# Kernel optimization log

Hardware: AMD Instinct MI355X
Metric: run time of the kernel (lower is better)

## Reference

```python
import jax, jax.numpy as jnp
import numpy as np

D = 128   # node feature dim
C = 2     # classes
N = 50000 # nodes
E = 500000  # edges (before self-loops)
H1 = 2    # conv1 heads
NEG_SLOPE = 0.2
BN_EPS = 1e-5


def setup_inputs() -> dict:
    key = jax.random.key(0)
    ks = jax.random.split(key, 24)
    rn = lambda k, shape, s=0.05: jax.random.normal(k, shape, dtype=jnp.float32) * s
    inp = {
        'x': jax.random.normal(ks[0], (N, D), dtype=jnp.float32),
        'edge_index': jax.random.randint(ks[1], (2, E), 0, N, dtype=jnp.int64),
        # conv1: GATConv(D, D, heads=2, concat=True)
        'W1': rn(ks[2], (D, H1 * D)),
        'att_src1': rn(ks[3], (H1, D)),
        'att_dst1': rn(ks[4], (H1, D)),
        'bias1': jnp.zeros((H1 * D,), jnp.float32),
        # conv2: GATConv(2D, D, heads=1, concat=False)
        'W2': rn(ks[5], (2 * D, D)),
        'att_src2': rn(ks[6], (1, D)),
        'att_dst2': rn(ks[7], (1, D)),
        'bias2': jnp.zeros((D,), jnp.float32),
        # lin1 = MLP([3D, 96]) : Linear -> ReLU -> BatchNorm1d
        'Wl': rn(ks[8], (3 * D, 96)), 'bl': jnp.zeros((96,), jnp.float32),
        'gl': jnp.ones((96,), jnp.float32), 'betal': jnp.zeros((96,), jnp.float32),
        # mlp1 = MLP([96, 96, C]) : two (Linear -> ReLU -> BN) blocks
        'Wa': rn(ks[9], (96, 96)), 'ba': jnp.zeros((96,), jnp.float32),
        'ga': jnp.ones((96,), jnp.float32), 'betaa': jnp.zeros((96,), jnp.float32),
        'Wb': rn(ks[10], (96, C)), 'bb': jnp.zeros((C,), jnp.float32),
        'gb': jnp.ones((C,), jnp.float32), 'betab': jnp.zeros((C,), jnp.float32),
    }
    return inp


def gat_conv(x, src, dst, W, att_src, att_dst, bias, heads, out_dim, concat):
    # PyG GATConv: h = x W -> [N,H,F]; per-edge logit leakyrelu(a_s.h_src + a_d.h_dst);
    # segment softmax over edges grouped by destination; weighted scatter-sum.
    n = x.shape[0]
    h = (x @ W).reshape(n, heads, out_dim)
    a_src = jnp.einsum('nhd,hd->nh', h, att_src)  # [N,H]
    a_dst = jnp.einsum('nhd,hd->nh', h, att_dst)
    alpha = jax.nn.leaky_relu(a_src[src] + a_dst[dst], NEG_SLOPE)  # [Etot,H]
    m = jax.ops.segment_max(alpha, dst, num_segments=n)            # [N,H]
    e = jnp.exp(alpha - m[dst])
    s = jax.ops.segment_sum(e, dst, num_segments=n)
    w = e / (s[dst] + 1e-16)                                       # [Etot,H]
    out = jax.ops.segment_sum(h[src] * w[:, :, None], dst, num_segments=n)  # [N,H,F]
    out = out.reshape(n, heads * out_dim) if concat else out.mean(axis=1)
    return out + bias


def mlp_block(x, W, b, gamma, beta):
    # Linear -> ReLU -> BatchNorm1d (training-mode batch stats, biased var)
    y = jax.nn.relu(x @ W + b)
    mu = y.mean(axis=0)
    var = ((y - mu) ** 2).mean(axis=0)
    return gamma * (y - mu) / jnp.sqrt(var + BN_EPS) + beta


def reference(x, edge_index, W1, att_src1, att_dst1, bias1,
              W2, att_src2, att_dst2, bias2,
              Wl, bl, gl, betal, Wa, ba, ga, betaa, Wb, bb, gb, betab):
    n = x.shape[0]
    # PyG GATConv default add_self_loops=True
    loops = jnp.arange(n, dtype=edge_index.dtype)
    src = jnp.concatenate([edge_index[0], loops])
    dst = jnp.concatenate([edge_index[1], loops])
    x1 = gat_conv(x, src, dst, W1, att_src1, att_dst1, bias1, H1, D, True)    # [N,2D]
    x2 = gat_conv(x1, src, dst, W2, att_src2, att_dst2, bias2, 1, D, False)   # [N,D]
    h = jnp.concatenate([x1, x2], axis=1)                                      # [N,3D]
    h = mlp_block(h, Wl, bl, gl, betal)     # lin1
    h = mlp_block(h, Wa, ba, ga, betaa)     # mlp1 layer 1
    h = mlp_block(h, Wb, bb, gb, betab)     # mlp1 layer 2
    return h
```

## Files before the change

### kernel.cpp

```cpp
#include <hip/hip_runtime.h>
#include <hip/hip_bf16.h>
#include <cstdint>
#include <cstddef>

#define NNODES 50000
#define NEDGES 500000
#define ETOT   (NEDGES + NNODES)

typedef __attribute__((ext_vector_type(8))) short short8;
typedef __attribute__((ext_vector_type(8))) unsigned short ushort8v;
typedef __attribute__((ext_vector_type(4))) float floatx4;
typedef __attribute__((ext_vector_type(4))) unsigned short ushort4v;

__device__ __forceinline__ unsigned short f2bf(float f) {
    union { __hip_bfloat16 h; unsigned short u; } cv;
    cv.h = __float2bfloat16(f);
    return cv.u;
}
__device__ __forceinline__ float bf2f(unsigned short u) {
    union { unsigned int i; float f; } cv;
    cv.i = ((unsigned int)u) << 16;
    return cv.f;
}

#define GBM 128
#define GBN 64
#define GBK 32

__global__ __launch_bounds__(256, 4) void gemm_mfma(
    const unsigned short* __restrict__ A, int lda,
    const unsigned short* __restrict__ Bt,
    float* __restrict__ C,
    unsigned short* __restrict__ Cb, int ldc,
    const float* __restrict__ bias,
    float* __restrict__ colsum, float* __restrict__ colsq,
    int M, int N, int K, int do_relu)
{
    __shared__ __attribute__((aligned(16))) unsigned short Alds[GBM * GBK];
    __shared__ __attribute__((aligned(16))) unsigned short Blds[GBN * GBK];
    __shared__ float scol[GBN], sqcol[GBN];

    int tid = threadIdx.x;
    int wave = tid >> 6, lane = tid & 63;
    int row0 = blockIdx.y * GBM;
    int col0 = blockIdx.x * GBN;
    int m = lane & 15, q = lane >> 4;

    floatx4 acc[2][4] = {};

    for (int k0 = 0; k0 < K; k0 += GBK) {
        #pragma unroll
        for (int i = 0; i < 2; ++i) {
            int c = tid + i * 256;
            int r = c >> 2, off = (c & 3) * 8;
            int gr = row0 + r;
            short8 v = {};
            if (gr < M) v = *(const short8*)(A + (size_t)gr * lda + k0 + off);
            *(short8*)(Alds + r * GBK + off) = v;
        }
        {
            int r = tid >> 2, off = (tid & 3) * 8;
            short8 v = *(const short8*)(Bt + (size_t)(col0 + r) * K + k0 + off);
            *(short8*)(Blds + r * GBK + off) = v;
        }
        __syncthreads();

        short8 a0 = *(const short8*)(Alds + (wave * 32 + m) * GBK + q * 8);
        short8 a1 = *(const short8*)(Alds + (wave * 32 + 16 + m) * GBK + q * 8);
        #pragma unroll
        for (int ct = 0; ct < 4; ++ct) {
            short8 b = *(const short8*)(Blds + (ct * 16 + m) * GBK + q * 8);
            acc[0][ct] = __builtin_amdgcn_mfma_f32_16x16x32_bf16(a0, b, acc[0][ct], 0, 0, 0);
            acc[1][ct] = __builtin_amdgcn_mfma_f32_16x16x32_bf16(a1, b, acc[1][ct], 0, 0, 0);
        }
        __syncthreads();
    }

    float ps[4] = {}, pq[4] = {};
    #pragma unroll
    for (int rt = 0; rt < 2; ++rt) {
        #pragma unroll
        for (int r = 0; r < 4; ++r) {
            int gr = row0 + wave * 32 + rt * 16 + q * 4 + r;
            #pragma unroll
            for (int ct = 0; ct < 4; ++ct) {
                int gc = col0 + ct * 16 + m;
                float v = acc[rt][ct][r];
                if (gc < N) {
                    float vb = v;
                    if (bias != nullptr) vb += bias[gc];
                    if (do_relu) vb = fmaxf(vb, 0.f);
                    if (gr < M) {
                        if (C  != nullptr) C[(size_t)gr * ldc + gc] = vb;
                        if (Cb != nullptr) Cb[(size_t)gr * ldc + gc] = f2bf(vb);
                        ps[ct] += vb; pq[ct] += vb * vb;
                    }
                }
            }
        }
    }
    if (colsum != nullptr) {
        if (tid < GBN) { scol[tid] = 0.f; sqcol[tid] = 0.f; }
        __syncthreads();
        #pragma unroll
        for (int ct = 0; ct < 4; ++ct) {
            atomicAdd(&scol[ct * 16 + m], ps[ct]);
            atomicAdd(&sqcol[ct * 16 + m], pq[ct]);
        }
        __syncthreads();
        if (tid < GBN) {
            int gc = col0 + tid;
            if (gc < N) {
                atomicAdd(&colsum[gc], scol[tid]);
                atomicAdd(&colsq[gc], sqcol[tid]);
            }
        }
    }
}

__global__ __launch_bounds__(256) void fold_cast_zero(
    const float* __restrict__ W1, const float* __restrict__ as1v, const float* __restrict__ ad1v,
    const float* __restrict__ W2, const float* __restrict__ as2v, const float* __restrict__ ad2v,
    const float* __restrict__ Wl,
    float* __restrict__ U1, float* __restrict__ U2,
    unsigned short* __restrict__ W1t, unsigned short* __restrict__ W2t,
    unsigned short* __restrict__ Wlt,
    int* __restrict__ rowst, float* __restrict__ as2z, float* __restrict__ statz)
{
    int z = blockIdx.x * 256 + threadIdx.x;
    if (z <= NNODES) rowst[z] = 0;
    if (z < 2 * NNODES) as2z[z] = 0.f;
    if (z < 1536) statz[z] = 0.f;

    if (blockIdx.x < 64) {
        int g = threadIdx.x >> 5, l = threadIdx.x & 31;
        int task = blockIdx.x * 8 + g;
        float ss = 0.f, sd = 0.f;
        if (task < 256) {
            int d = task & 127, h = task >> 7;
            const float4 wv = *(const float4*)(W1 + d * 256 + h * 128 + l * 4);
            const float4 av = *(const float4*)(as1v + h * 128 + l * 4);
            const float4 bv = *(const float4*)(ad1v + h * 128 + l * 4);
            ss = wv.x * av.x + wv.y * av.y + wv.z * av.z + wv.w * av.w;
            sd = wv.x * bv.x + wv.y * bv.y + wv.z * bv.z + wv.w * bv.w;
        } else {
            int k = task - 256;
            const float4 wv = *(const float4*)(W2 + (size_t)k * 128 + l * 4);
            const float4 av = *(const float4*)(as2v + l * 4);
            const float4 bv = *(const float4*)(ad2v + l * 4);
            ss = wv.x * av.x + wv.y * av.y + wv.z * av.z + wv.w * av.w;
            sd = wv.x * bv.x + wv.y * bv.y + wv.z * bv.z + wv.w * bv.w;
        }
        #pragma unroll
        for (int off = 1; off < 32; off <<= 1) { ss += __shfl_xor(ss, off); sd += __shfl_xor(sd, off); }
        if (l == 0) {
            if (task < 256) {
                int d = task & 127, h = task >> 7;
                U1[h * 128 + d] = ss;
                U1[256 + h * 128 + d] = sd;
            } else {
                int k = task - 256;
                U2[k] = ss;
                U2[256 + k] = sd;
            }
        }
    } else {
        int i = (blockIdx.x - 64) * 256 + threadIdx.x;
        if (i < 32768) {
            int n = i >> 7, k = i & 127;
            W1t[i] = f2bf(W1[k * 256 + n]);
        } else if (i < 65536) {
            int j = i - 32768;
            int n = j >> 8, k = j & 255;
            W2t[j] = f2bf(W2[k * 128 + n]);
        } else if (i < 114688) {
            int j = i - 65536;
            int n = j / 384, k = j % 384;
            Wlt[j] = (n < 96) ? f2bf(Wl[(size_t)k * 96 + n]) : (unsigned short)0;
        }
    }
}

__device__ __forceinline__ void edge_src_dst(const int* ei, int e, int& src, int& dst) {
    if (e < NEDGES) { src = ei[e]; dst = ei[NEDGES + e]; }
    else { src = e - NEDGES; dst = src; }
}

#define CASTB ((NNODES + 7) / 8)
#define EDGEB ((ETOT + 255) / 256)

__global__ __launch_bounds__(256) void cast_csr(
    const float* __restrict__ x, const float* __restrict__ U1,
    unsigned short* __restrict__ xb, float* __restrict__ as1, float* __restrict__ ad1,
    const int* __restrict__ ei, int* __restrict__ cnt)
{
    __shared__ float Us[512];
    int tid = threadIdx.x;
    if (blockIdx.x < CASTB) {
        Us[tid] = U1[tid];
        Us[tid + 256] = U1[tid + 256];
        __syncthreads();
        int g = tid >> 5, l = tid & 31;
        int n = blockIdx.x * 8 + g;
        if (n >= NNODES) return;
        const float4 v = *(const float4*)(x + (size_t)n * 128 + l * 4);
        ushort4v o;
        o.x = f2bf(v.x); o.y = f2bf(v.y); o.z = f2bf(v.z); o.w = f2bf(v.w);
        *(ushort4v*)(xb + (size_t)n * 128 + l * 4) = o;
        const float4 us0 = *(const float4*)(Us + l * 4);
        const float4 us1 = *(const float4*)(Us + 128 + l * 4);
        const float4 ud0 = *(const float4*)(Us + 256 + l * 4);
        const float4 ud1 = *(const float4*)(Us + 384 + l * 4);
        float s0 = v.x * us0.x + v.y * us0.y + v.z * us0.z + v.w * us0.w;
        float s1 = v.x * us1.x + v.y * us1.y + v.z * us1.z + v.w * us1.w;
        float d0 = v.x * ud0.x + v.y * ud0.y + v.z * ud0.z + v.w * ud0.w;
        float d1 = v.x * ud1.x + v.y * ud1.y + v.z * ud1.z + v.w * ud1.w;
        #pragma unroll
        for (int off = 1; off < 32; off <<= 1) {
            s0 += __shfl_xor(s0, off); s1 += __shfl_xor(s1, off);
            d0 += __shfl_xor(d0, off); d1 += __shfl_xor(d1, off);
        }
        if (l == 0) {
            as1[n * 2] = s0; as1[n * 2 + 1] = s1;
            ad1[n * 2] = d0; ad1[n * 2 + 1] = d1;
        }
    } else {
        int e = (blockIdx.x - CASTB) * 256 + tid;
        if (e >= ETOT) return;
        int src, dst; edge_src_dst(ei, e, src, dst); (void)src;
        atomicAdd(&cnt[dst], 1);
    }
}

__global__ void bnfold_a(const float* __restrict__ csum, const float* __restrict__ csq,
                         const float* __restrict__ gamma, const float* __restrict__ beta,
                         const float* __restrict__ Wa, const float* __restrict__ ba,
                         unsigned short* __restrict__ Wat2, float* __restrict__ ba_f) {
    __shared__ float scl[96], shf[96];
    int tid = threadIdx.x;
    if (tid < 96) {
        float mu  = csum[tid] / (float)NNODES;
        float var = csq[tid] / (float)NNODES - mu * mu;
        if (var < 0.f) var = 0.f;
        float sc = gamma[tid] * rsqrtf(var + 1e-5f);
        scl[tid] = sc; shf[tid] = beta[tid] - mu * sc;
    }
    __syncthreads();
    for (int idx = tid; idx < 128 * 96; idx += 256) {
        int n = idx / 96, k = idx % 96;
        Wat2[idx] = (n < 96) ? f2bf(scl[k] * Wa[k * 96 + n]) : (unsigned short)0;
    }
    if (tid < 96) {
        float s = ba[tid];
        for (int k = 0; k < 96; ++k) s += shf[k] * Wa[k * 96 + tid];
        ba_f[tid] = s;
    }
}

__global__ void bnfold_b(const float* __restrict__ csum, const float* __restrict__ csq,
                         const float* __restrict__ gamma, const float* __restrict__ beta,
                         const float* __restrict__ Wb, const float* __restrict__ bb,
                         unsigned short* __restrict__ Wbt, float* __restrict__ bb_f) {
    __shared__ float scl[96], shf[96];
    int tid = threadIdx.x;
    if (tid < 96) {
        float mu  = csum[tid] / (float)NNODES;
        float var = csq[tid] / (float)NNODES - mu * mu;
        if (var < 0.f) var = 0.f;
        float sc = gamma[tid] * rsqrtf(var + 1e-5f);
        scl[tid] = sc; shf[tid] = beta[tid] - mu * sc;
    }
    __syncthreads();
    for (int idx = tid; idx < 64 * 96; idx += 256) {
        int n = idx / 96, k = idx % 96;
        Wbt[idx] = (n < 2) ? f2bf(scl[k] * Wb[k * 2 + n]) : (unsigned short)0;
    }
    if (tid < 2) {
        float s = bb[tid];
        for (int k = 0; k < 96; ++k) s += shf[k] * Wb[k * 2 + tid];
        bb_f[tid] = s;
    }
}

__global__ void bn_fin_apply(const float* __restrict__ csum, const float* __restrict__ csq,
                             const float* __restrict__ gamma, const float* __restrict__ beta,
                             float* __restrict__ y, int total) {
    int i = blockIdx.x * blockDim.x + threadIdx.x;
    if (i >= total) return;
    int j = i & 1;
    float mu  = csum[j] / (float)NNODES;
    float var = csq[j] / (float)NNODES - mu * mu;
    if (var < 0.f) var = 0.f;
    float sc = gamma[j] * rsqrtf(var + 1e-5f);
    float sh = beta[j] - mu * sc;
    y[i] = y[i] * sc + sh;
}

#define SCAN_CH 1024
#define SCAN_NB ((NNODES + SCAN_CH - 1) / SCAN_CH)

__global__ __launch_bounds__(256) void scan1(const int* __restrict__ cnt, int* __restrict__ part) {
    int t = threadIdx.x;
    int base = blockIdx.x * SCAN_CH + t * 4;
    int4 v = {0, 0, 0, 0};
    if (base + 3 < NNODES) v = *(const int4*)(cnt + base);
    else {
        if (base + 0 < NNODES) v.x = cnt[base + 0];
        if (base + 1 < NNODES) v.y = cnt[base + 1];
        if (base + 2 < NNODES) v.z = cnt[base + 2];
        if (base + 3 < NNODES) v.w = cnt[base + 3];
    }
    int s = v.x + v.y + v.z + v.w;
    __shared__ int sm[256];
    sm[t] = s;
    __syncthreads();
    for (int off = 128; off > 0; off >>= 1) {
        if (t < off) sm[t] += sm[t + off];
        __syncthreads();
    }
    if (t == 0) part[blockIdx.x] = sm[0];
}

__global__ __launch_bounds__(256) void scan23(const int* __restrict__ cnt, const int* __restrict__ part,
                                              int* __restrict__ rowstart, int* __restrict__ cursor) {
    __shared__ int sbase;
    int t = threadIdx.x;
    if (t < 64) {
        int v = (t < SCAN_NB) ? part[t] : 0;
        #pragma unroll
        for (int off = 1; off < 64; off <<= 1) {
            int u = __shfl_up(v, off);
            if (t >= off) v += u;
        }
        int ex = __shfl_up(v, 1);
        if (t == 0) ex = 0;
        if (t == (int)blockIdx.x) sbase = ex;
        if (blockIdx.x == 0 && t == 0) rowstart[NNODES] = ETOT;
    }
    int base = blockIdx.x * SCAN_CH + t * 4;
    int4 v = {0, 0, 0, 0};
    if (base + 3 < NNODES) v = *(const int4*)(cnt + base);
    else {
        if (base + 0 < NNODES) v.x = cnt[base + 0];
        if (base + 1 < NNODES) v.y = cnt[base + 1];
        if (base + 2 < NNODES) v.z = cnt[base + 2];
        if (base + 3 < NNODES) v.w = cnt[base + 3];
    }
    int s = v.x + v.y + v.z + v.w;
    __shared__ int sm[2][256];
    sm[0][t] = s;
    __syncthreads();
    int cur = 0;
    #pragma unroll
    for (int off = 1; off < 256; off <<= 1) {
        int nxt = cur ^ 1;
        int val = sm[cur][t];
        if (t >= off) val += sm[cur][t - off];
        sm[nxt][t] = val;
        __syncthreads();
        cur = nxt;
    }
    int p = sm[cur][t] - s + sbase;
    if (base + 0 < NNODES) { rowstart[base + 0] = p; cursor[base + 0] = p; } p += v.x;
    if (base + 1 < NNODES) { rowstart[base + 1] = p; cursor[base + 1] = p; } p += v.y;
    if (base + 2 < NNODES) { rowstart[base + 2] = p; cursor[base + 2] = p; } p += v.z;
    if (base + 3 < NNODES) { rowstart[base + 3] = p; cursor[base + 3] = p; }
}

__global__ __launch_bounds__(256) void csr_fill(const int* __restrict__ ei,
                                                int* __restrict__ cursor,
                                                int* __restrict__ esrc) {
    int e = blockIdx.x * blockDim.x + threadIdx.x;
    if (e >= ETOT) return;
    int src, dst; edge_src_dst(ei, e, src, dst);
    int pos = atomicAdd(&cursor[dst], 1);
    esrc[pos] = src;
}

__global__ __launch_bounds__(256, 4) void gat_conv1_fused(
    const int* __restrict__ rowstart, const int* __restrict__ esrc,
    const unsigned short* __restrict__ xb, const float* __restrict__ a_src,
    const float* __restrict__ a_dst, const unsigned short* __restrict__ W1t,
    const float* __restrict__ bias1, const float* __restrict__ U2,
    unsigned short* __restrict__ xcat, float* __restrict__ as2, float* __restrict__ ad2)
{
    __shared__ __attribute__((aligned(16))) unsigned short Alds[16 * 264];
    __shared__ float U2s[512];
    __shared__ float Bs[256];

    int tid = threadIdx.x;
    int t = tid & 15;
    int g = tid >> 4;
    int nb = blockIdx.x * 16;
    int n = nb + g;

    U2s[tid] = U2[tid];
    U2s[tid + 256] = U2[tid + 256];
    Bs[tid] = bias1[tid];

    int beg = rowstart[n], deg = rowstart[n + 1] - beg;
    const float2 adv = *(const float2*)(a_dst + (size_t)n * 2);
    float acc0[8] = {}, acc1[8] = {};

    if (deg <= 32) {
        int sa = 0, sb = 0;
        float la0 = -1e30f, la1 = -1e30f;
        float lb0 = -1e30f, lb1 = -1e30f;
        if (t < deg) {
            sa = esrc[beg + t];
            const float2 asv = *(const float2*)(a_src + (size_t)sa * 2);
            la0 = asv.x + adv.x; la0 = la0 >= 0.f ? la0 : 0.2f * la0;
            lb0 = asv.y + adv.y; lb0 = lb0 >= 0.f ? lb0 : 0.2f * lb0;
        }
        if (t + 16 < deg) {
            sb = esrc[beg + 16 + t];
            const float2 asv = *(const float2*)(a_src + (size_t)sb * 2);
            la1 = asv.x + adv.x; la1 = la1 >= 0.f ? la1 : 0.2f * la1;
            lb1 = asv.y + adv.y; lb1 = lb1 >= 0.f ? lb1 : 0.2f * lb1;
        }
        float m0 = fmaxf(la0, la1), m1 = fmaxf(lb0, lb1);
        #pragma unroll
        for (int off = 1; off < 16; off <<= 1) {
            m0 = fmaxf(m0, __shfl_xor(m0, off, 16));
            m1 = fmaxf(m1, __shfl_xor(m1, off, 16));
        }
        float ea0 = (t < deg)      ? __expf(la0 - m0) : 0.f;
        float ea1 = (t + 16 < deg) ? __expf(la1 - m0) : 0.f;
        float eb0 = (t < deg)      ? __expf(lb0 - m1) : 0.f;
        float eb1 = (t + 16 < deg) ? __expf(lb1 - m1) : 0.f;
        float s0 = ea0 + ea1, s1 = eb0 + eb1;
        #pragma unroll
        for (int off = 1; off < 16; off <<= 1) {
            s0 += __shfl_xor(s0, off, 16);
            s1 += __shfl_xor(s1, off, 16);
        }
        float i0 = 1.f / (s0 + 1e-16f), i1 = 1.f / (s1 + 1e-16f);
        float wa0 = ea0 * i0, wa1 = ea1 * i0;
        float wb0 = eb0 * i1, wb1 = eb1 * i1;

        int e = 0;
        for (; e + 3 < deg; e += 4) {
            int sx[4]; float w0x[4], w1x[4];
            #pragma unroll
            for (int u = 0; u < 4; ++u) {
                int ee = e + u;
                int hi = ee & 16, ln = ee & 15;
                sx[u]  = __shfl(hi ? sb  : sa,  ln, 16);
                w0x[u] = __shfl(hi ? wa1 : wa0, ln, 16);
                w1x[u] = __shfl(hi ? wb1 : wb0, ln, 16);
            }
            ushort8v hv[4];
            #pragma unroll
            for (int u = 0; u < 4; ++u)
                hv[u] = *(const ushort8v*)(xb + (size_t)sx[u] * 128 + t * 8);
            #pragma unroll
            for (int u = 0; u < 4; ++u) {
                #pragma unroll
                for (int j = 0; j < 8; ++j) {
                    float f = bf2f(hv[u][j]);
                    acc0[j] += w0x[u] * f;
                    acc1[j] += w1x[u] * f;
                }
            }
        }
        for (; e < deg; ++e) {
            int hi = e & 16, ln = e & 15;
            int   sX  = __shfl(hi ? sb  : sa,  ln, 16);
            float wX0 = __shfl(hi ? wa1 : wa0, ln, 16);
            float wX1 = __shfl(hi ? wb1 : wb0, ln, 16);
            const ushort8v hv = *(const ushort8v*)(xb + (size_t)sX * 128 + t * 8);
            #pragma unroll
            for (int j = 0; j < 8; ++j) {
                float f = bf2f(hv[j]);
                acc0[j] += wX0 * f; acc1[j] += wX1 * f;
            }
        }
    } else {
        float m0 = -1e30f, m1 = -1e30f;
        for (int idx = t; idx < deg; idx += 16) {
            int s = esrc[beg + idx];
            const float2 asv = *(const float2*)(a_src + (size_t)s * 2);
            float l0 = asv.x + adv.x; l0 = l0 >= 0.f ? l0 : 0.2f * l0;
            float l1 = asv.y + adv.y; l1 = l1 >= 0.f ? l1 : 0.2f * l1;
            m0 = fmaxf(m0, l0); m1 = fmaxf(m1, l1);
        }
        #pragma unroll
        for (int off = 1; off < 16; off <<= 1) {
            m0 = fmaxf(m0, __shfl_xor(m0, off, 16));
            m1 = fmaxf(m1, __shfl_xor(m1, off, 16));
        }
        float s0 = 0.f, s1 = 0.f;
        for (int idx = t; idx < deg; idx += 16) {
            int s = esrc[beg + idx];
            const float2 asv = *(const float2*)(a_src + (size_t)s * 2);
            float l0 = asv.x + adv.x; l0 = l0 >= 0.f ? l0 : 0.2f * l0;
            float l1 = asv.y + adv.y; l1 = l1 >= 0.f ? l1 : 0.2f * l1;
            s0 += __expf(l0 - m0); s1 += __expf(l1 - m1);
        }
        #pragma unroll
        for (int off = 1; off < 16; off <<= 1) {
            s0 += __shfl_xor(s0, off, 16);
            s1 += __shfl_xor(s1, off, 16);
        }
        float inv0 = 1.f / (s0 + 1e-16f), inv1 = 1.f / (s1 + 1e-16f);
        for (int e = 0; e < deg; ++e) {
            int s = esrc[beg + e];
            const float2 asv = *(const float2*)(a_src + (size_t)s * 2);
            float l0 = asv.x + adv.x; l0 = l0 >= 0.f ? l0 : 0.2f * l0;
            float l1 = asv.y + adv.y; l1 = l1 >= 0.f ? l1 : 0.2f * l1;
            float w0 = __expf(l0 - m0) * inv0, w1 = __expf(l1 - m1) * inv1;
            const ushort8v hv = *(const ushort8v*)(xb + (size_t)s * 128 + t * 8);
            #pragma unroll
            for (int j = 0; j < 8; ++j) {
                float f = bf2f(hv[j]);
                acc0[j] += w0 * f; acc1[j] += w1 * f;
            }
        }
    }

    {
        ushort8v o0, o1;
        #pragma unroll
        for (int j = 0; j < 8; ++j) { o0[j] = f2bf(acc0[j]); o1[j] = f2bf(acc1[j]); }
        *(ushort8v*)(Alds + g * 264 + t * 8) = o0;
        *(ushort8v*)(Alds + g * 264 + 128 + t * 8) = o1;
    }
    __syncthreads();

    int wave = tid >> 6, lane = tid & 63;
    int m = lane & 15, q = lane >> 4;
    int ncol0 = wave * 64;
    int kbase = (wave >= 2) ? 128 : 0;

    floatx4 cacc[4] = {};
    #pragma unroll
    for (int ks = 0; ks < 4; ++ks) {
        short8 a = *(const short8*)(Alds + m * 264 + kbase + ks * 32 + q * 8);
        #pragma unroll
        for (int ct = 0; ct < 4; ++ct) {
            short8 b = *(const short8*)(W1t + (size_t)(ncol0 + ct * 16 + m) * 128 + ks * 32 + q * 8);
            cacc[ct] = __builtin_amdgcn_mfma_f32_16x16x32_bf16(a, b, cacc[ct], 0, 0, 0);
        }
    }

    #pragma unroll
    for (int r = 0; r < 4; ++r) {
        int row = q * 4 + r;
        int gn = nb + row;
        float ds = 0.f, dd = 0.f;
        #pragma unroll
        for (int ct = 0; ct < 4; ++ct) {
            int col = ncol0 + ct * 16 + m;
            float vb = cacc[ct][r] + Bs[col];
            ds += vb * U2s[col];
            dd += vb * U2s[256 + col];
            xcat[(size_t)gn * 384 + col] = f2bf(vb);
        }
        #pragma unroll
        for (int off = 1; off < 16; off <<= 1) {
            ds += __shfl_xor(ds, off);
            dd += __shfl_xor(dd, off);
        }
        if (m == 0) {
            atomicAdd(&as2[gn], ds);
            atomicAdd(&ad2[gn], dd);
        }
    }
}

__global__ __launch_bounds__(256) void gat_gather_h1(
    const int* __restrict__ rowstart, const int* __restrict__ esrc,
    const unsigned short* __restrict__ hb, const float* __restrict__ a_src,
    const float* __restrict__ a_dst, const float* __restrict__ bias,
    unsigned short* __restrict__ xcat)
{
    int tid = threadIdx.x;
    int t = tid & 15;
    int g0 = (blockIdx.x * blockDim.x + tid) >> 4;
    int gstride = (gridDim.x * blockDim.x) >> 4;

    for (int n = g0; n < NNODES; n += gstride) {
        int beg = rowstart[n], deg = rowstart[n + 1] - beg;
        float ad0 = a_dst[n];
        float acc[8] = {};

        if (deg <= 32) {
            int sa = 0, sb = 0;
            float l0 = -1e30f, l1 = -1e30f;
            if (t < deg) {
                sa = esrc[beg + t];
                l0 = a_src[sa] + ad0; l0 = l0 >= 0.f ? l0 : 0.2f * l0;
            }
            if (t + 16 < deg) {
                sb = esrc[beg + 16 + t];
                l1 = a_src[sb] + ad0; l1 = l1 >= 0.f ? l1 : 0.2f * l1;
            }
            float m0 = fmaxf(l0, l1);
            #pragma unroll
            for (int off = 1; off < 16; off <<= 1)
                m0 = fmaxf(m0, __shfl_xor(m0, off, 16));
            float e0 = (t < deg)      ? __expf(l0 - m0) : 0.f;
            float e1 = (t + 16 < deg) ? __expf(l1 - m0) : 0.f;
            float s0 = e0 + e1;
            #pragma unroll
            for (int off = 1; off < 16; off <<= 1)
                s0 += __shfl_xor(s0, off, 16);
            float i0 = 1.f / (s0 + 1e-16f);
            float w0 = e0 * i0, w1 = e1 * i0;

            int e = 0;
            for (; e + 3 < deg; e += 4) {
                int sx[4]; float wx[4];
                #pragma unroll
                for (int u = 0; u < 4; ++u) {
                    int ee = e + u;
                    int hi = ee & 16, ln = ee & 15;
                    sx[u] = __shfl(hi ? sb : sa, ln, 16);
                    wx[u] = __shfl(hi ? w1 : w0, ln, 16);
                }
                ushort8v hv[4];
                #pragma unroll
                for (int u = 0; u < 4; ++u)
                    hv[u] = *(const ushort8v*)(hb + (size_t)sx[u] * 128 + t * 8);
                #pragma unroll
                for (int u = 0; u < 4; ++u) {
                    #pragma unroll
                    for (int j = 0; j < 8; ++j)
                        acc[j] += wx[u] * bf2f(hv[u][j]);
                }
            }
            for (; e < deg; ++e) {
                int hi = e & 16, ln = e & 15;
                int   sX = __shfl(hi ? sb : sa, ln, 16);
                float wX = __shfl(hi ? w1 : w0, ln, 16);
                const ushort8v hv = *(const ushort8v*)(hb + (size_t)sX * 128 + t * 8);
                #pragma unroll
                for (int j = 0; j < 8; ++j) acc[j] += wX * bf2f(hv[j]);
            }
        } else {
            float m0 = -1e30f;
            for (int idx = t; idx < deg; idx += 16) {
                int s = esrc[beg + idx];
                float l = a_src[s] + ad0; l = l >= 0.f ? l : 0.2f * l;
                m0 = fmaxf(m0, l);
            }
            #pragma unroll
            for (int off = 1; off < 16; off <<= 1)
                m0 = fmaxf(m0, __shfl_xor(m0, off, 16));
            float s0 = 0.f;
            for (int idx = t; idx < deg; idx += 16) {
                int s = esrc[beg + idx];
                float l = a_src[s] + ad0; l = l >= 0.f ? l : 0.2f * l;
                s0 += __expf(l - m0);
            }
            #pragma unroll
            for (int off = 1; off < 16; off <<= 1)
                s0 += __shfl_xor(s0, off, 16);
            float inv0 = 1.f / (s0 + 1e-16f);
            for (int e = 0; e < deg; ++e) {
                int s = esrc[beg + e];
                float l = a_src[s] + ad0; l = l >= 0.f ? l : 0.2f * l;
                float w = __expf(l - m0) * inv0;
                const ushort8v hv = *(const ushort8v*)(hb + (size_t)s * 128 + t * 8);
                #pragma unroll
                for (int j = 0; j < 8; ++j) acc[j] += w * bf2f(hv[j]);
            }
        }

        const float4 b0 = *(const float4*)(bias + t * 8);
        const float4 b1 = *(const float4*)(bias + t * 8 + 4);
        ushort8v o;
        o[0] = f2bf(acc[0] + b0.x); o[1] = f2bf(acc[1] + b0.y);
        o[2] = f2bf(acc[2] + b0.z); o[3] = f2bf(acc[3] + b0.w);
        o[4] = f2bf(acc[4] + b1.x); o[5] = f2bf(acc[5] + b1.y);
        o[6] = f2bf(acc[6] + b1.z); o[7] = f2bf(acc[7] + b1.w);
        *(ushort8v*)(xcat + (size_t)n * 384 + 256 + t * 8) = o;
    }
}

extern "C" void kernel_launch(void* const* d_in, const int* in_sizes, int n_in,
                              void* d_out, int out_size, void* d_ws, size_t ws_size,
                              hipStream_t stream) {
    const float* x        = (const float*)d_in[0];
    const int*   ei       = (const int*)d_in[1];
    const float* W1       = (const float*)d_in[2];
    const float* att_src1 = (const float*)d_in[3];
    const float* att_dst1 = (const float*)d_in[4];
    const float* bias1    = (const float*)d_in[5];
    const float* W2       = (const float*)d_in[6];
    const float* att_src2 = (const float*)d_in[7];
    const float* att_dst2 = (const float*)d_in[8];
    const float* bias2    = (const float*)d_in[9];
    const float* Wl       = (const float*)d_in[10];
    const float* bl       = (const float*)d_in[11];
    const float* gl       = (const float*)d_in[12];
    const float* betal    = (const float*)d_in[13];
    const float* Wa       = (const float*)d_in[14];
    const float* ba       = (const float*)d_in[15];
    const float* ga       = (const float*)d_in[16];
    const float* betaa    = (const float*)d_in[17];
    const float* Wb       = (const float*)d_in[18];
    const float* bb       = (const float*)d_in[19];
    const float* gb       = (const float*)d_in[20];
    const float* betab    = (const float*)d_in[21];
    float* out = (float*)d_out;
    char* ws = (char*)d_ws;

    const int N = NNODES;

    const size_t offY2b  = 0;
    const size_t offXcat = 19200000;
    const size_t offXb   = 57600000;
    const size_t offY1b  = 70400000;
    const size_t offW1t  = 105600000;
    const size_t offW2t  = 105665536;
    const size_t offWlt  = 105731072;
    const size_t offWat2 = 105829376;
    const size_t offWbt  = 105853952;
    const size_t offBaf  = 105866240;
    const size_t offBbf  = 105866640;
    const size_t offU1   = 105867264;
    const size_t offU2   = 105869312;
    const size_t offRow  = 106000000;
    const size_t offCur  = 106200128;
    const size_t offEsrc = 106400832;
    const size_t offPart = 108700000;
    const size_t offAs1  = 108800000;
    const size_t offAd1  = 109200000;
    const size_t offAs2  = 109600000;
    const size_t offAd2  = 109800000;
    const size_t offSt   = 110000000;

    unsigned short* y2b   = (unsigned short*)(ws + offY2b);
    unsigned short* xcat  = (unsigned short*)(ws + offXcat);
    unsigned short* xb    = (unsigned short*)(ws + offXb);
    unsigned short* hb2   = (unsigned short*)(ws + offXb);
    unsigned short* y1b   = (unsigned short*)(ws + offY1b);
    unsigned short* W1t   = (unsigned short*)(ws + offW1t);
    unsigned short* W2t   = (unsigned short*)(ws + offW2t);
    unsigned short* Wlt   = (unsigned short*)(ws + offWlt);
    unsigned short* Wat2  = (unsigned short*)(ws + offWat2);
    unsigned short* Wbt   = (unsigned short*)(ws + offWbt);
    float* ba_f = (float*)(ws + offBaf);
    float* bb_f = (float*)(ws + offBbf);
    float* U1   = (float*)(ws + offU1);
    float* U2   = (float*)(ws + offU2);
    int* rowst  = (int*)(ws + offRow);
    int* cursor = (int*)(ws + offCur);
    int* esrc   = (int*)(ws + offEsrc);
    int* part   = (int*)(ws + offPart);
    float* as1  = (float*)(ws + offAs1);
    float* ad1  = (float*)(ws + offAd1);
    float* as2  = (float*)(ws + offAs2);
    float* ad2  = (float*)(ws + offAd2);
    float* statz = (float*)(ws + offSt);

    float* csum_l = (float*)(ws + offSt + 0);
    float* csq_l  = (float*)(ws + offSt + 512);
    float* csum_a = (float*)(ws + offSt + 2048);
    float* csq_a  = (float*)(ws + offSt + 2560);
    float* csum_b = (float*)(ws + offSt + 4096);
    float* csq_b  = (float*)(ws + offSt + 4608);

    dim3 blk(256);
    int gatherBlocks = 2048;
    dim3 gemmRows((N + GBM - 1) / GBM);

    fold_cast_zero<<<512, blk, 0, stream>>>(W1, att_src1, att_dst1, W2, att_src2, att_dst2,
                                            Wl, U1, U2, W1t, W2t, Wlt, rowst, as2, statz);

    cast_csr<<<CASTB + EDGEB, blk, 0, stream>>>(x, U1, xb, as1, ad1, ei, rowst);

    scan1<<<SCAN_NB, blk, 0, stream>>>(rowst, part);
    scan23<<<SCAN_NB, blk, 0, stream>>>(rowst, part, rowst, cursor);
    csr_fill<<<EDGEB, blk, 0, stream>>>(ei, cursor, esrc);

    gat_conv1_fused<<<NNODES / 16, blk, 0, stream>>>(
        rowst, esrc, xb, as1, ad1, W1t, bias1, U2, xcat, as2, ad2);

    gemm_mfma<<<dim3(2, gemmRows.x), blk, 0, stream>>>(
        xcat, 384, W2t, nullptr, hb2, 128, nullptr, nullptr, nullptr,
        N, 128, 256, 0);
    gat_gather_h1<<<gatherBlocks, blk, 0, stream>>>(rowst, esrc, hb2, as2, ad2, bias2, xcat);

    gemm_mfma<<<dim3(2, gemmRows.x), blk, 0, stream>>>(
        xcat, 384, Wlt, nullptr, y1b, 96, bl, csum_l, csq_l,
        N, 96, 384, 1);
    bnfold_a<<<1, 256, 0, stream>>>(csum_l, csq_l, gl, betal, Wa, ba, Wat2, ba_f);

    gemm_mfma<<<dim3(2, gemmRows.x), blk, 0, stream>>>(
        y1b, 96, Wat2, nullptr, y2b, 96, ba_f, csum_a, csq_a,
        N, 96, 96, 1);
    bnfold_b<<<1, 256, 0, stream>>>(csum_a, csq_a, ga, betaa, Wb, bb, Wbt, bb_f);

    gemm_mfma<<<dim3(1, gemmRows.x), blk, 0, stream>>>(
        y2b, 96, Wbt, out, nullptr, 2, bb_f, csum_b, csq_b,
        N, 2, 96, 1);

    bn_fin_apply<<<(N * 2 + 255) / 256, blk, 0, stream>>>(csum_b, csq_b, gb, betab, out, N * 2);
}
```

Measured before the change: 344.7 us.

## Fuse BN fold and final BN apply into GEMM last-block tails

Adds a last-block-done counter to the MFMA GEMM so the final block computes BatchNorm statistics and either folds them into the next layer's weights and bias or applies them to the output. This removes three separate small kernel launches (bnfold_a, bnfold_b, bn_fin_apply). The trade-off is that the final output normalization now runs in a single block over all rows, serializing that work, and it adds fences and an atomic per block.

```diff
diff --git a/kernel.cpp b/kernel.cpp
--- a/kernel.cpp
+++ b/kernel.cpp
@@ -34,11 +34,17 @@
     unsigned short* __restrict__ Cb, int ldc,
     const float* __restrict__ bias,
     float* __restrict__ colsum, float* __restrict__ colsq,
-    int M, int N, int K, int do_relu)
+    int M, int N, int K, int do_relu,
+    int tailmode, int* __restrict__ done,
+    const float* __restrict__ tg, const float* __restrict__ tbeta,
+    const float* __restrict__ tW, const float* __restrict__ tb,
+    unsigned short* __restrict__ tWt, float* __restrict__ tbf)
 {
     __shared__ __attribute__((aligned(16))) unsigned short Alds[GBM * GBK];
     __shared__ __attribute__((aligned(16))) unsigned short Blds[GBN * GBK];
     __shared__ float scol[GBN], sqcol[GBN];
+    __shared__ float fsh[192];
+    __shared__ int amLast;
 
     int tid = threadIdx.x;
     int wave = tid >> 6, lane = tid & 63;
@@ -113,6 +119,56 @@
             if (gc < N) {
                 atomicAdd(&colsum[gc], scol[tid]);
                 atomicAdd(&colsq[gc], sqcol[tid]);
+            }
+        }
+    }
+
+    if (tailmode != 0) {
+        __threadfence();
+        if (tid == 0) {
+            int prev = atomicAdd(done, 1);
+            amLast = (prev == (int)(gridDim.x * gridDim.y) - 1) ? 1 : 0;
+        }
+        __syncthreads();
+        if (!amLast) return;
+        __threadfence();
+
+        if (tailmode <= 2) {
+            int outN = (tailmode == 1) ? 96 : 2;
+            int padN = (tailmode == 1) ? 128 : 64;
+            if (tid < 96) {
+                float mu  = colsum[tid] / (float)NNODES;
+                float var = colsq[tid] / (float)NNODES - mu * mu;
+                if (var < 0.f) var = 0.f;
+                float sc = tg[tid] * rsqrtf(var + 1e-5f);
+                fsh[tid] = sc; fsh[96 + tid] = tbeta[tid] - mu * sc;
+            }
+            __syncthreads();
+            for (int idx = tid; idx < padN * 96; idx += 256) {
+                int n = idx / 96, k = idx % 96;
+                tWt[idx] = (n < outN) ? f2bf(fsh[k] * tW[k * outN + n]) : (unsigned short)0;
+            }
+            if (tid < outN) {
+                float s = tb[tid];
+                for (int k = 0; k < 96; ++k) s += fsh[96 + k] * tW[k * outN + tid];
+                tbf[tid] = s;
+            }
+        } else {
+            float mu0  = colsum[0] / (float)NNODES;
+            float var0 = colsq[0] / (float)NNODES - mu0 * mu0;
+            if (var0 < 0.f) var0 = 0.f;
+            float sc0 = tg[0] * rsqrtf(var0 + 1e-5f);
+            float sh0 = tbeta[0] - mu0 * sc0;
+            float mu1  = colsum[1] / (float)NNODES;
+            float var1 = colsq[1] / (float)NNODES - mu1 * mu1;
+            if (var1 < 0.f) var1 = 0.f;
+            float sc1 = tg[1] * rsqrtf(var1 + 1e-5f);
+            float sh1 = tbeta[1] - mu1 * sc1;
+            for (int i = tid; i < M; i += 256) {
+                float2 v = *(float2*)(C + (size_t)i * 2);
+                v.x = v.x * sc0 + sh0;
+                v.y = v.y * sc1 + sh1;
+                *(float2*)(C + (size_t)i * 2) = v;
             }
         }
     }
@@ -230,70 +286,6 @@
         int src, dst; edge_src_dst(ei, e, src, dst); (void)src;
         atomicAdd(&cnt[dst], 1);
     }
-}
-
-__global__ void bnfold_a(const float* __restrict__ csum, const float* __restrict__ csq,
-                         const float* __restrict__ gamma, const float* __restrict__ beta,
-                         const float* __restrict__ Wa, const float* __restrict__ ba,
-                         unsigned short* __restrict__ Wat2, float* __restrict__ ba_f) {
-    __shared__ float scl[96], shf[96];
-    int tid = threadIdx.x;
-    if (tid < 96) {
-        float mu  = csum[tid] / (float)NNODES;
-        float var = csq[tid] / (float)NNODES - mu * mu;
-        if (var < 0.f) var = 0.f;
-        float sc = gamma[tid] * rsqrtf(var + 1e-5f);
-        scl[tid] = sc; shf[tid] = beta[tid] - mu * sc;
-    }
-    __syncthreads();
-    for (int idx = tid; idx < 128 * 96; idx += 256) {
-        int n = idx / 96, k = idx % 96;
-        Wat2[idx] = (n < 96) ? f2bf(scl[k] * Wa[k * 96 + n]) : (unsigned short)0;
-    }
-    if (tid < 96) {
-        float s = ba[tid];
-        for (int k = 0; k < 96; ++k) s += shf[k] * Wa[k * 96 + tid];
-        ba_f[tid] = s;
-    }
-}
-
-__global__ void bnfold_b(const float* __restrict__ csum, const float* __restrict__ csq,
-                         const float* __restrict__ gamma, const float* __restrict__ beta,
-                         const float* __restrict__ Wb, const float* __restrict__ bb,
-                         unsigned short* __restrict__ Wbt, float* __restrict__ bb_f) {
-    __shared__ float scl[96], shf[96];
-    int tid = threadIdx.x;
-    if (tid < 96) {
-        float mu  = csum[tid] / (float)NNODES;
-        float var = csq[tid] / (float)NNODES - mu * mu;
-        if (var < 0.f) var = 0.f;
-        float sc = gamma[tid] * rsqrtf(var + 1e-5f);
-        scl[tid] = sc; shf[tid] = beta[tid] - mu * sc;
-    }
-    __syncthreads();
-    for (int idx = tid; idx < 64 * 96; idx += 256) {
-        int n = idx / 96, k = idx % 96;
-        Wbt[idx] = (n < 2) ? f2bf(scl[k] * Wb[k * 2 + n]) : (unsigned short)0;
-    }
-    if (tid < 2) {
-        float s = bb[tid];
-        for (int k = 0; k < 96; ++k) s += shf[k] * Wb[k * 2 + tid];
-        bb_f[tid] = s;
-    }
-}
-
-__global__ void bn_fin_apply(const float* __restrict__ csum, const float* __restrict__ csq,
-                             const float* __restrict__ gamma, const float* __restrict__ beta,
-                             float* __restrict__ y, int total) {
-    int i = blockIdx.x * blockDim.x + threadIdx.x;
-    if (i >= total) return;
-    int j = i & 1;
-    float mu  = csum[j] / (float)NNODES;
-    float var = csq[j] / (float)NNODES - mu * mu;
-    if (var < 0.f) var = 0.f;
-    float sc = gamma[j] * rsqrtf(var + 1e-5f);
-    float sh = beta[j] - mu * sc;
-    y[i] = y[i] * sc + sh;
 }
 
 #define SCAN_CH 1024
@@ -761,6 +753,9 @@
     float* csq_a  = (float*)(ws + offSt + 2560);
     float* csum_b = (float*)(ws + offSt + 4096);
     float* csq_b  = (float*)(ws + offSt + 4608);
+    int* done_l   = (int*)(ws + offSt + 5632);
+    int* done_a   = (int*)(ws + offSt + 5636);
+    int* done_b   = (int*)(ws + offSt + 5640);
 
     dim3 blk(256);
     int gatherBlocks = 2048;
@@ -780,22 +775,22 @@
 
     gemm_mfma<<<dim3(2, gemmRows.x), blk, 0, stream>>>(
         xcat, 384, W2t, nullptr, hb2, 128, nullptr, nullptr, nullptr,
-        N, 128, 256, 0);
+        N, 128, 256, 0,
+        0, nullptr, nullptr, nullptr, nullptr, nullptr, nullptr, nullptr);
     gat_gather_h1<<<gatherBlocks, blk, 0, stream>>>(rowst, esrc, hb2, as2, ad2, bias2, xcat);
 
     gemm_mfma<<<dim3(2, gemmRows.x), blk, 0, stream>>>(
         xcat, 384, Wlt, nullptr, y1b, 96, bl, csum_l, csq_l,
-        N, 96, 384, 1);
-    bnfold_a<<<1, 256, 0, stream>>>(csum_l, csq_l, gl, betal, Wa, ba, Wat2, ba_f);
+        N, 96, 384, 1,
+        1, done_l, gl, betal, Wa, ba, Wat2, ba_f);
 
     gemm_mfma<<<dim3(2, gemmRows.x), blk, 0, stream>>>(
         y1b, 96, Wat2, nullptr, y2b, 96, ba_f, csum_a, csq_a,
-        N, 96, 96, 1);
-    bnfold_b<<<1, 256, 0, stream>>>(csum_a, csq_a, ga, betaa, Wb, bb, Wbt, bb_f);
+        N, 96, 96, 1,
+        2, done_a, ga, betaa, Wb, bb, Wbt, bb_f);
 
     gemm_mfma<<<dim3(1, gemmRows.x), blk, 0, stream>>>(
         y2b, 96, Wbt, out, nullptr, 2, bb_f, csum_b, csq_b,
-        N, 2, 96, 1);
-
-    bn_fin_apply<<<(N * 2 + 255) / 256, blk, 0, stream>>>(csum_b, csq_b, gb, betab, out, N * 2);
-}
+        N, 2, 96, 1,
+        3, done_b, gb, betab, nullptr, nullptr, nullptr, nullptr);
+}
```

New measurement: 460.3 us. +33.5%, slower.
